# Kernel tuning notes

Measured on AMD Instinct MI355X. Metric: run time of the kernel, lower is better.

The kernel has to match this reference:

```python
import jax, jax.numpy as jnp
import numpy as np
from jax import lax

B, T, D = 256, 512, 256          # batch, time, input_dim (neurons)
HE, HC, HG = 256, 256, 256       # encoder/controller/generator hidden
L, F = 64, 64                    # latent_dim, factor_dim


def gru_cell(x, h, Wih, Whh, bih, bhh):
    # PyTorch GRU gate order: r, z, n
    gi = x @ Wih.T + bih
    gh = h @ Whh.T + bhh
    ir, iz, inn = jnp.split(gi, 3, axis=-1)
    hr, hz, hn = jnp.split(gh, 3, axis=-1)
    r = jax.nn.sigmoid(ir + hr)
    z = jax.nn.sigmoid(iz + hz)
    n = jnp.tanh(inn + r * hn)
    return (1.0 - z) * n + z * h


def setup_inputs() -> dict:
    key = jax.random.key(0)
    ks = iter(jax.random.split(key, 40))
    def p(shape, scale=0.05):
        return (jax.random.normal(next(ks), shape, dtype=jnp.float32) * scale)
    inp = {
        "x": jax.random.normal(next(ks), (B, T, D), dtype=jnp.float32),
        "eps_u": jax.random.normal(next(ks), (T, B, L), dtype=jnp.float32),
        # bidirectional encoder GRU (forward / backward directions)
        "Wih_ef": p((3 * HE, D)), "Whh_ef": p((3 * HE, HE)), "bih_ef": p((3 * HE,)), "bhh_ef": p((3 * HE,)),
        "Wih_eb": p((3 * HE, D)), "Whh_eb": p((3 * HE, HE)), "bih_eb": p((3 * HE,)), "bhh_eb": p((3 * HE,)),
        # initial-condition heads
        "W_mu0": p((L, 2 * HE)), "b_mu0": p((L,)), "W_lv0": p((L, 2 * HE)), "b_lv0": p((L,)),
        # controller GRU + heads
        "Wih_c": p((3 * HC, D + F)), "Whh_c": p((3 * HC, HC)), "bih_c": p((3 * HC,)), "bhh_c": p((3 * HC,)),
        "W_cmu": p((L, HC)), "b_cmu": p((L,)), "W_clv": p((L, HC)), "b_clv": p((L,)),
        # generator GRU
        "Wih_g": p((3 * HG, L)), "Whh_g": p((3 * HG, HG)), "bih_g": p((3 * HG,)), "bhh_g": p((3 * HG,)),
        # readouts
        "W_f": p((F, HG)), "b_f": p((F,)), "W_r": p((D, F)), "b_r": p((D,)),
    }
    return inp


def reference(x, eps_u, Wih_ef, Whh_ef, bih_ef, bhh_ef, Wih_eb, Whh_eb, bih_eb, bhh_eb,
              W_mu0, b_mu0, W_lv0, b_lv0, Wih_c, Whh_c, bih_c, bhh_c,
              W_cmu, b_cmu, W_clv, b_clv, Wih_g, Whh_g, bih_g, bhh_g,
              W_f, b_f, W_r, b_r):
    xt = jnp.transpose(x, (1, 0, 2))  # [T, B, D]
    h0 = jnp.zeros((x.shape[0], HE), dtype=x.dtype)

    def enc_f(h, x_t):
        return gru_cell(x_t, h, Wih_ef, Whh_ef, bih_ef, bhh_ef), None

    def enc_b(h, x_t):
        return gru_cell(x_t, h, Wih_eb, Whh_eb, bih_eb, bhh_eb), None

    h_fwd, _ = lax.scan(enc_f, h0, xt)
    h_bwd, _ = lax.scan(enc_b, h0, xt, reverse=True)
    h_enc = jnp.concatenate([h_fwd, h_bwd], axis=-1)  # [B, 2*HE]

    mu0 = h_enc @ W_mu0.T + b_mu0
    lv0 = h_enc @ W_lv0.T + b_lv0
    kl_ics = (0.5 * jnp.sum(jnp.exp(lv0) + mu0 ** 2 - 1.0 - lv0, axis=1)).mean()
    # note: z0 is sampled in the original but never used (generator starts from zeros)

    c0 = jnp.zeros((x.shape[0], HC), dtype=x.dtype)
    g0 = jnp.zeros((x.shape[0], HG), dtype=x.dtype)
    f0 = jnp.zeros((x.shape[0], F), dtype=x.dtype)

    def step(carry, inputs):
        c_h, g_h, prev_f = carry
        x_t, eps_t = inputs
        c_in = jnp.concatenate([x_t, prev_f], axis=-1)  # [B, D+F]
        c_h = gru_cell(c_in, c_h, Wih_c, Whh_c, bih_c, bhh_c)
        mu_u = c_h @ W_cmu.T + b_cmu
        lv_u = c_h @ W_clv.T + b_clv
        u_t = mu_u + eps_t * jnp.exp(0.5 * lv_u)
        kl_t = (0.5 * jnp.sum(jnp.exp(lv_u) + mu_u ** 2 - 1.0 - lv_u, axis=1)).mean()
        g_h = gru_cell(u_t, g_h, Wih_g, Whh_g, bih_g, bhh_g)
        factors = g_h @ W_f.T + b_f
        rates_t = jnp.exp(factors @ W_r.T + b_r)
        return (c_h, g_h, factors), (rates_t, factors, kl_t)

    _, (rates, factors_all, kl_ts) = lax.scan(step, (c0, g0, f0), (xt, eps_u))
    rates = jnp.transpose(rates, (1, 0, 2))           # [B, T, D]
    factors_all = jnp.transpose(factors_all, (1, 0, 2))  # [B, T, F]
    kl_ctrl = kl_ts.mean()  # sum of per-step means / T
    return (rates, kl_ics, kl_ctrl, factors_all)
```

## Files before the change

### kernel.cpp

```cpp
#include <hip/hip_runtime.h>

typedef unsigned char u8;
typedef unsigned short u16;
typedef unsigned int u32;
typedef unsigned long long u64;
typedef short short8 __attribute__((ext_vector_type(8)));
typedef __bf16 bf16x8 __attribute__((ext_vector_type(8)));
typedef float f32x4 __attribute__((ext_vector_type(4)));
typedef float f32x2 __attribute__((ext_vector_type(2)));
typedef long longx2 __attribute__((ext_vector_type(2)));

#define DEV static __device__ __forceinline__

struct Params {
  const float *x, *eps;
  const float *Wih_ef, *Whh_ef, *bih_ef, *bhh_ef;
  const float *Wih_eb, *Whh_eb, *bih_eb, *bhh_eb;
  const float *W_mu0, *b_mu0, *W_lv0, *b_lv0;
  const float *Wih_c, *Whh_c, *bih_c, *bhh_c;
  const float *W_cmu, *b_cmu, *W_clv, *b_clv;
  const float *Wih_g, *Whh_g, *bih_g, *bhh_g;
  const float *W_f, *b_f, *W_r, *b_r;
  u8  *Xf8;
  u16 *ebf;
  u16 *wihcbf;
  float *bfc;
  u8 *wihef8, *whhef8, *wiheb8, *whheb8;
  u8 *whhc8, *whhg8;
  u8 *wihcf8, *wihg8;
  u8 *wf8, *wcmu8, *wclv8;
  u16 *wrbf;
  float *cbn;
  float *gb;
  float *hdb;
  float *fb2;
  float *eb;
  float *henc;
  float *klacc;
  float *klics;
  u8 *Gxc;
  float *out;
};

constexpr size_t RATES_N = 33554432ull;
constexpr size_t FOUT    = RATES_N + 2ull;

DEV u16 f2bf(float x) {
  unsigned u = __builtin_bit_cast(unsigned, x);
  u = (u + 0x7FFFu + ((u >> 16) & 1u)) >> 16;
  return (u16)u;
}
DEV float bf2f(u32 s) { return __builtin_bit_cast(float, s << 16); }
DEV unsigned f2e4m3(float x) {
  unsigned u = __builtin_bit_cast(unsigned, x);
  unsigned s = (u >> 24) & 0x80u;
  float ax = __builtin_bit_cast(float, u & 0x7FFFFFFFu);
  if (ax > 448.f) return s | 0x7E;
  if (ax < 0.0009765625f) return s;
  if (ax < 0.015625f) {
    int m = (int)rintf(ax * 512.f);
    if (m >= 8) return s | 0x08;
    return s | (unsigned)m;
  }
  unsigned au = __builtin_bit_cast(unsigned, ax);
  int E = (int)(au >> 23) - 127;
  unsigned m = au & 0x7FFFFFu;
  unsigned r = (m + 0x7FFFFu + ((m >> 20) & 1u)) >> 20;
  if (r >= 8) { r = 0; ++E; if (E > 8) return s | 0x7E; }
// ... 48 lines not shown
}
DEV short8 ldfrag(const u16* p0, int stride) {
  const int l = threadIdx.x & 63;
  const u16* p = p0 + (size_t)(l & 15) * stride + ((l >> 4) << 3);
  return *reinterpret_cast<const short8*>(p);
}
DEV short8 ldfrag_f32(const float* p0, int stride) {
  const int l = threadIdx.x & 63;
  const float* p = p0 + (size_t)(l & 15) * stride + ((l >> 4) << 3);
  f32x4 a = *reinterpret_cast<const f32x4*>(p);
  f32x4 b = *reinterpret_cast<const f32x4*>(p + 4);
  short8 r;
  r[0]=(short)f2bf(a[0]); r[1]=(short)f2bf(a[1]); r[2]=(short)f2bf(a[2]); r[3]=(short)f2bf(a[3]);
  r[4]=(short)f2bf(b[0]); r[5]=(short)f2bf(b[1]); r[6]=(short)f2bf(b[2]); r[7]=(short)f2bf(b[3]);
  return r;
}
DEV longx2 ldws2(const u8* w, int tile, int p) {
  return *(const longx2*)(w + ((size_t)tile << 12) + (p << 10) + ((threadIdx.x & 63) << 4));
}
DEV longx2 ldws64x(const u8* w, int tile) {
  return *(const longx2*)(w + ((size_t)tile << 10) + ((threadIdx.x & 63) << 4));
}
DEV int fragoff(int row, int jb) { return jb * 128 + ((row ^ (jb & 15)) << 3); }
DEV long ldsF(const u8* m, int r0, int rs, int kk) {
  int l = threadIdx.x & 63;
  int jb = kk * 4 + (l >> 4);
  return *(const long*)(m + ((r0 >> 4) << (rs + 4)) + fragoff(l & 15, jb));
}
DEV void stF(u8* m, int row, int col, unsigned v) {
  *(unsigned*)(m + fragoff(row, col >> 3) + (col & 7)) = v;
}
DEV short8 ldsB16(const u8* m, int r0, int kk) {
  int l = threadIdx.x & 63;
  int row = r0 + (l & 15);
  int off = row * 512 + kk * 64 + ((l >> 4) << 4);
  off ^= (row & 7) << 4;
  return *(const short8*)(m + off);
}
DEV void stage16(u8* dst, const u8* src, int nbytes) {
  for (int i = threadIdx.x * 16; i < nbytes; i += blockDim.x * 16) {
    int row = i >> 9;
    int off = i ^ ((row & 7) << 4);
    *(f32x4*)(dst + off) = *(const f32x4*)(src + i);
  }
}

__global__ __launch_bounds__(256) void k_init(Params P) {
  const size_t g  = (size_t)blockIdx.x * 256 + threadIdx.x;
  const size_t gs = (size_t)gridDim.x * 256;
  for (size_t i = g; i < 4194304ull; i += gs) {
    size_t flat = i << 3;
    int b = (int)(flat >> 17);
    int rem = (int)(flat & 131071);
    int t = rem >> 8, d = rem & 255;
    *(u64*)(P.Xf8 + (((size_t)t * 256 + b) << 8) + d) = pack8f8(P.x + flat);
  }
  for (size_t o = g; o < 1048576ull; o += gs) {
    int l = (int)(o & 63), k2 = (int)((o >> 6) & 1);
    int bt = (int)((o >> 7) & 15), t = (int)(o >> 11);
    int row = bt * 16 + (l & 15), col = k2 * 32 + ((l >> 4) << 3);
    const float* s = P.eps + ((size_t)t * 256 + row) * 64 + col;
    f32x4 v0 = *(const f32x4*)s, v1 = *(const f32x4*)(s + 4);
    short8 ob;
    ob[0]=(short)f2bf(v0[0]); ob[1]=(short)f2bf(v0[1]); ob[2]=(short)f2bf(v0[2]); ob[3]=(short)f2bf(v0[3]);
    ob[4]=(short)f2bf(v1[0]); ob[5]=(short)f2bf(v1[1]); ob[6]=(short)f2bf(v1[2]); ob[7]=(short)f2bf(v1[3]);
    *(short8*)((u8*)P.ebf + o * 16) = ob;
  }
  const int gi = (int)g, gsi = (int)gs;
  for (int i = gi; i < 24576; i += gsi) {
    int l = i & 63, kk = (i >> 6) & 7, tile = i >> 9;
    int row = tile * 16 + (l & 15), col = kk * 32 + ((l >> 4) << 3);
    size_t so = (size_t)row * 256 + col;
    size_t db = ((size_t)tile << 12) + ((kk >> 1) << 10) + (l << 4) + ((kk & 1) << 3);
    *(u64*)(P.whhc8  + db) = pack8f8(P.Whh_c  + so);
    *(u64*)(P.whhg8  + db) = pack8f8(P.Whh_g  + so);
    *(u64*)(P.wihef8 + db) = pack8f8(P.Wih_ef + so);
    *(u64*)(P.whhef8 + db) = pack8f8(P.Whh_ef + so);
    *(u64*)(P.wiheb8 + db) = pack8f8(P.Wih_eb + so);
    *(u64*)(P.whheb8 + db) = pack8f8(P.Whh_eb + so);
  }
  for (int i = gi; i < 2048; i += gsi) {
    int l = i & 63, kk = (i >> 6) & 7, tile = i >> 9;
    int row = tile * 16 + (l & 15), col = kk * 32 + ((l >> 4) << 3);
    size_t so = (size_t)row * 256 + col;
    size_t db = ((size_t)tile << 12) + ((kk >> 1) << 10) + (l << 4) + ((kk & 1) << 3);
    *(u64*)(P.wf8   + db) = pack8f8(P.W_f   + so);
    *(u64*)(P.wcmu8 + db) = pack8f8(P.W_cmu + so);
    *(u64*)(P.wclv8 + db) = pack8f8(P.W_clv + so);
  }
  for (int i = gi; i < 6144; i += gsi) {
    int l = i & 63, k2 = (i >> 6) & 1, tile = i >> 7;
    int row = tile * 16 + (l & 15), col = k2 * 32 + ((l >> 4) << 3);
    size_t db = ((size_t)tile << 10) + (l << 4) + (k2 << 3);
    *(u64*)(P.wihcf8 + db) = pack8f8(P.Wih_c + (size_t)row * 320 + 256 + col);
    *(u64*)(P.wihg8  + db) = pack8f8(P.Wih_g + (size_t)row * 64 + col);
  }
  for (int i = gi; i < 196608; i += gsi) {
    int r = i >> 8, c = i & 255;
    P.wihcbf[i] = f2bf(P.Wih_c[r * 320 + c]);
  }
  for (int i = gi; i < 16384; i += gsi) P.wrbf[i] = f2bf(P.W_r[i]);
  for (int i = gi; i < 768; i += gsi)
    P.bfc[i] = P.bih_c[i] + (i < 512 ? P.bhh_c[i] : 0.f);
  for (int i = gi; i < 256; i += gsi) {
    P.cbn[i] = P.bhh_c[512 + i];
    P.gb[i]        = P.bih_g[i] + P.bhh_g[i];
    P.gb[256 + i]  = P.bih_g[256 + i] + P.bhh_g[256 + i];
    P.gb[512 + i]  = P.bih_g[512 + i];
    P.gb[768 + i]  = P.bhh_g[512 + i];
    P.eb[i]        = P.bih_ef[i] + P.bhh_ef[i];
    P.eb[256 + i]  = P.bih_ef[256 + i] + P.bhh_ef[256 + i];
    P.eb[512 + i]  = P.bih_ef[512 + i];
    P.eb[768 + i]  = P.bhh_ef[512 + i];
    P.eb[1024 + i] = P.bih_eb[i] + P.bhh_eb[i];
    P.eb[1280 + i] = P.bih_eb[256 + i] + P.bhh_eb[256 + i];
    P.eb[1536 + i] = P.bih_eb[512 + i];
    P.eb[1792 + i] = P.bhh_eb[512 + i];
  }
  for (int i = gi; i < 128; i += gsi) P.hdb[i] = (i < 64) ? P.b_cmu[i] : P.b_clv[i - 64];
  for (int i = gi; i < 64; i += gsi)  P.fb2[i] = P.b_f[i];
}

__global__ __launch_bounds__(512, 2) void k_gx(Params P) {
  extern __shared__ char smem[];
  u8* sA = (u8*)smem;
  u8* sB = sA + 65536;
  const int nc = blockIdx.x % 6;
  const int tb = blockIdx.x / 6;
  const int t = tb >> 1, bh = tb & 1;
  stage16(sA, (const u8*)(P.wihcbf + (size_t)nc * 128 * 256), 65536);
  for (int i = threadIdx.x * 8; i < 32768; i += 512 * 8) {
    int r = i >> 8, c = i & 255;
    const float* s = P.x + ((size_t)(bh * 128 + r) * 512 + t) * 256 + c;
    f32x4 v0 = *(const f32x4*)s, v1 = *(const f32x4*)(s + 4);
    short8 o;
    o[0]=(short)f2bf(v0[0]); o[1]=(short)f2bf(v0[1]); o[2]=(short)f2bf(v0[2]); o[3]=(short)f2bf(v0[3]);
    o[4]=(short)f2bf(v1[0]); o[5]=(short)f2bf(v1[1]); o[6]=(short)f2bf(v1[2]); o[7]=(short)f2bf(v1[3]);
    int off = (r * 512 + c * 2) ^ ((r & 7) << 4);
    *(short8*)(sB + off) = o;
  }
  __syncthreads();
  const int lane = threadIdx.x & 63, wid = threadIdx.x >> 6;
  const int rq = (lane >> 4) << 2;
  const int nglob = nc * 128 + wid * 16;
  short8 Af[8];
  #pragma unroll
  for (int kk = 0; kk < 8; ++kk) Af[kk] = ldsB16(sA, wid * 16, kk);
  float bq[4];
  #pragma unroll
  for (int q = 0; q < 4; ++q) bq[q] = P.bfc[nglob + rq + q];
  #pragma unroll 1
  for (int bt = 0; bt < 8; ++bt) {
    f32x4 acc = {0.f, 0.f, 0.f, 0.f};
    #pragma unroll
    for (int kk = 0; kk < 8; ++kk)
      acc = MFMA(Af[kk], ldsB16(sB, bt * 16, kk), acc);
    float v0 = acc[0] + bq[0], v1 = acc[1] + bq[1], v2 = acc[2] + bq[2], v3 = acc[3] + bq[3];
    unsigned pw = pk2fp8<false>(v0, v1, 0u); pw = pk2fp8<true>(v2, v3, pw);
    *(u32*)(P.Gxc + (((size_t)(t * 16 + bh * 8 + bt) * 48 + (nglob >> 4)) << 8) + (lane << 2)) = pw;
  }
}

DEV void cg_role(const Params& P, int blk, char* smem) {
  u8* hc8  = (u8*)smem;
  u8* hg8  = hc8 + 8192;
  u8* f8b  = hg8 + 8192;
  float* sml  = (float*)(f8b + 2048);
  float* sred = sml + 16 * 132;

  const int lane = threadIdx.x & 63, wid = threadIdx.x >> 6;
  const int cl = lane & 15, rq = (lane >> 4) << 2;
  const int b0 = blk << 4, j0 = wid << 5, jt = wid << 1;
  const int sel = wid >> 2, l0 = (wid & 3) << 4;

  for (int i = threadIdx.x * 4; i < 18432; i += 512 * 4) *(int*)(hc8 + i) = 0;

  f32x4 bnv[2], brv[2], bzv[2], biv[2], bhv2[2];
  #pragma unroll
  for (int c2 = 0; c2 < 2; ++c2) {
    int j = j0 + c2 * 16 + rq;
    bnv[c2]  = *(const f32x4*)(P.cbn + j);
    brv[c2]  = *(const f32x4*)(P.gb + j);
    bzv[c2]  = *(const f32x4*)(P.gb + 256 + j);
    biv[c2]  = *(const f32x4*)(P.gb + 512 + j);
    bhv2[c2] = *(const f32x4*)(P.gb + 768 + j);
  }
  f32x4 hbv = *(const f32x4*)(P.hdb + sel * 64 + l0 + rq);
  f32x4 fbv = {0, 0, 0, 0};
  if (wid < 4) fbv = *(const f32x4*)(P.fb2 + wid * 16 + rq);

  f32x4 hcM[2] = {{0,0,0,0},{0,0,0,0}};
  f32x4 hgM[2] = {{0,0,0,0},{0,0,0,0}};
  float klv = 0.f;
  __syncthreads();

  #pragma unroll 1
  for (int t = 0; t < 512; ++t) {
    const int cur = t & 1, prv = cur ^ 1;
    u8 *hcP = hc8 + prv * 4096, *hcC = hc8 + cur * 4096;
    u8 *hgP = hg8 + prv * 4096, *hgC = hg8 + cur * 4096;
    int zz = 0; asm volatile("" : "+v"(zz));
    const u8* wcS = P.whhc8 + zz;
    const u8* wgS = P.whhg8 + zz;
    const u8* cfS = P.wihcf8 + zz;
    const u8* guS = P.wihg8 + zz;
    const u8* hdS = (sel ? P.wclv8 : P.wcmu8) + zz;
    const u8* wfS = P.wf8 + zz;
    u32 gx[6];
    { const u8* gp = P.Gxc + (((size_t)(t * 16 + blk) * 48) << 8) + (lane << 2);
      #pragma unroll
      for (int c2 = 0; c2 < 2; ++c2)
        #pragma unroll
        for (int g3 = 0; g3 < 3; ++g3)
          gx[c2 * 3 + g3] = *(const u32*)(gp + ((g3 * 16 + jt + c2) << 8));
    }
    short8 ee0 = *(const short8*)((const u8*)P.ebf + (((size_t)(t * 16 + blk) * 2 + 0) << 10) + lane * 16);
    short8 ee1 = *(const short8*)((const u8*)P.ebf + (((size_t)(t * 16 + blk) * 2 + 1) << 10) + lane * 16);
    long hf[8];
    #pragma unroll
    for (int kk = 0; kk < 8; ++kk) hf[kk] = ldsF(hcP, 0, 8, kk);
    long ff0 = ldsF(f8b + prv * 1024, 0, 6, 0);
    long ff1 = ldsF(f8b + prv * 1024, 0, 6, 1);
    #pragma unroll
    for (int c2 = 0; c2 < 2; ++c2) {
      longx2 w0[4], w1[4], w2[4];
      #pragma unroll
      for (int p = 0; p < 4; ++p) {
        w0[p] = ldws2(wcS,      jt + c2, p);
        w1[p] = ldws2(wcS, 16 + jt + c2, p);
        w2[p] = ldws2(wcS, 32 + jt + c2, p);
      }
      longx2 cf0 = ldws64x(cfS,      jt + c2);
      longx2 cf1 = ldws64x(cfS, 16 + jt + c2);
      longx2 cf2 = ldws64x(cfS, 32 + jt + c2);
      f32x4 ar = {0,0,0,0}, az = {0,0,0,0}, ai = {0,0,0,0}, ah = {0,0,0,0};
      #pragma unroll
      for (int p = 0; p < 4; ++p) {
        ar = mfma8(w0[p].x, hf[2*p], ar);  ar = mfma8(w0[p].y, hf[2*p+1], ar);
        az = mfma8(w1[p].x, hf[2*p], az);  az = mfma8(w1[p].y, hf[2*p+1], az);
        ah = mfma8(w2[p].x, hf[2*p], ah);  ah = mfma8(w2[p].y, hf[2*p+1], ah);
      }
      ar = mfma8(cf0.x, ff0, ar); ar = mfma8(cf0.y, ff1, ar);
      az = mfma8(cf1.x, ff0, az); az = mfma8(cf1.y, ff1, az);
      ai = mfma8(cf2.x, ff0, ai); ai = mfma8(cf2.y, ff1, ai);
      f32x2 rlo = pkf32<false>(gx[c2*3+0]), rhi = pkf32<true>(gx[c2*3+0]);
      f32x2 zlo = pkf32<false>(gx[c2*3+1]), zhi = pkf32<true>(gx[c2*3+1]);
      f32x2 nlo = pkf32<false>(gx[c2*3+2]), nhi = pkf32<true>(gx[c2*3+2]);
      f32x4 bn = bnv[c2];
      float h0 = gru_h(ar[0]+rlo[0], az[0]+zlo[0], ai[0]+nlo[0], ah[0]+bn[0], hcM[c2][0]);
      float h1 = gru_h(ar[1]+rlo[1], az[1]+zlo[1], ai[1]+nlo[1], ah[1]+bn[1], hcM[c2][1]);
      float h2 = gru_h(ar[2]+rhi[0], az[2]+zhi[0], ai[2]+nhi[0], ah[2]+bn[2], hcM[c2][2]);
      float h3 = gru_h(ar[3]+rhi[1], az[3]+zhi[1], ai[3]+nhi[1], ah[3]+bn[3], hcM[c2][3]);
      hcM[c2][0] = h0; hcM[c2][1] = h1; hcM[c2][2] = h2; hcM[c2][3] = h3;
      unsigned pw = pk2fp8<false>(h0, h1, 0u); pw = pk2fp8<true>(h2, h3, pw);
      stF(hcC, cl, j0 + c2 * 16 + rq, pw);
    }
    __syncthreads();
    { long hcv[8];
      #pragma unroll
      for (int kk = 0; kk < 8; ++kk) hcv[kk] = ldsF(hcC, 0, 8, kk);
      f32x4 am = {0,0,0,0};
      #pragma unroll
      for (int p = 0; p < 4; ++p) {
        longx2 wp = ldws2(hdS, wid & 3, p);
        am = mfma8(wp.x, hcv[2*p], am);
        am = mfma8(wp.y, hcv[2*p+1], am);
      }
      am += hbv;
      *(f32x4*)(sml + cl * 132 + sel * 64 + l0 + rq) = am;
    }
    __syncthreads();
    long U[2];
    { const float* ml = sml + cl * 132;
      const int kh = (lane >> 4) << 3;
      #pragma unroll
      for (int k2 = 0; k2 < 2; ++k2) {
        f32x4 mu0 = *(const f32x4*)(ml + k2 * 32 + kh);
        f32x4 mu1 = *(const f32x4*)(ml + k2 * 32 + kh + 4);
        f32x4 lv0 = *(const f32x4*)(ml + 64 + k2 * 32 + kh);
        f32x4 lv1 = *(const f32x4*)(ml + 64 + k2 * 32 + kh + 4);
        short8 ev = k2 ? ee1 : ee0;
        float uu[8];
        #pragma unroll
        for (int e = 0; e < 4; ++e) {
          float epv = bf2f((u32)(u16)ev[e]);
          uu[e] = mu0[e] + epv * __expf(0.5f * lv0[e]);
        }
        #pragma unroll
        for (int e = 0; e < 4; ++e) {
          float epv = bf2f((u32)(u16)ev[4 + e]);
          uu[4 + e] = mu1[e] + epv * __expf(0.5f * lv1[e]);
        }
        unsigned pa = pk2fp8<false>(uu[0], uu[1], 0u); pa = pk2fp8<true>(uu[2], uu[3], pa);
        unsigned pb = pk2fp8<false>(uu[4], uu[5], 0u); pb = pk2fp8<true>(uu[6], uu[7], pb);
        U[k2] = (long)(((u64)pb << 32) | (u64)pa);
      }
    }
    long hg[8];
    #pragma unroll
    for (int kk = 0; kk < 8; ++kk) hg[kk] = ldsF(hgP, 0, 8, kk);
    #pragma unroll
    for (int c2 = 0; c2 < 2; ++c2) {
      longx2 g0[4], g1[4], g2[4];
      #pragma unroll
      for (int p = 0; p < 4; ++p) {
        g0[p] = ldws2(wgS,      jt + c2, p);
        g1[p] = ldws2(wgS, 16 + jt + c2, p);
        g2[p] = ldws2(wgS, 32 + jt + c2, p);
      }
      longx2 u0 = ldws64x(guS,      jt + c2);
      longx2 u1 = ldws64x(guS, 16 + jt + c2);
      longx2 u2 = ldws64x(guS, 32 + jt + c2);
      f32x4 gr = {0,0,0,0}, gz = {0,0,0,0}, gi = {0,0,0,0}, gh = {0,0,0,0};
      #pragma unroll
      for (int p = 0; p < 4; ++p) {
        gr = mfma8(g0[p].x, hg[2*p], gr);  gr = mfma8(g0[p].y, hg[2*p+1], gr);
        gz = mfma8(g1[p].x, hg[2*p], gz);  gz = mfma8(g1[p].y, hg[2*p+1], gz);
        gh = mfma8(g2[p].x, hg[2*p], gh);  gh = mfma8(g2[p].y, hg[2*p+1], gh);
      }
      gr = mfma8(u0.x, U[0], gr); gr = mfma8(u0.y, U[1], gr);
      gz = mfma8(u1.x, U[0], gz); gz = mfma8(u1.y, U[1], gz);
      gi = mfma8(u2.x, U[0], gi); gi = mfma8(u2.y, U[1], gi);
      float h0 = gru_h(gr[0]+brv[c2][0], gz[0]+bzv[c2][0], gi[0]+biv[c2][0], gh[0]+bhv2[c2][0], hgM[c2][0]);
      float h1 = gru_h(gr[1]+brv[c2][1], gz[1]+bzv[c2][1], gi[1]+biv[c2][1], gh[1]+bhv2[c2][1], hgM[c2][1]);
      float h2 = gru_h(gr[2]+brv[c2][2], gz[2]+bzv[c2][2], gi[2]+biv[c2][2], gh[2]+bhv2[c2][2], hgM[c2][2]);
      float h3 = gru_h(gr[3]+brv[c2][3], gz[3]+bzv[c2][3], gi[3]+biv[c2][3], gh[3]+bhv2[c2][3], hgM[c2][3]);
      hgM[c2][0] = h0; hgM[c2][1] = h1; hgM[c2][2] = h2; hgM[c2][3] = h3;
      unsigned pw = pk2fp8<false>(h0, h1, 0u); pw = pk2fp8<true>(h2, h3, pw);
      stF(hgC, cl, j0 + c2 * 16 + rq, pw);
    }
    __syncthreads();
    if (wid < 4) {
      long hgv[8];
      #pragma unroll
      for (int kk = 0; kk < 8; ++kk) hgv[kk] = ldsF(hgC, 0, 8, kk);
      f32x4 af = {0,0,0,0};
      #pragma unroll
      for (int p = 0; p < 4; ++p) {
        longx2 wp = ldws2(wfS, wid, p);
        af = mfma8(wp.x, hgv[2*p], af);
        af = mfma8(wp.y, hgv[2*p+1], af);
      }
      af += fbv;
      float* fo = P.out + FOUT + (size_t)(b0 + cl) * 32768 + (size_t)t * 64 + wid * 16 + rq;
      f32x2 lo = {af[0], af[1]}, hi2 = {af[2], af[3]};
      *(f32x2*)fo = lo;
      *(f32x2*)(fo + 2) = hi2;
      unsigned pw = pk2fp8<false>(af[0], af[1], 0u); pw = pk2fp8<true>(af[2], af[3], pw);
      stF(f8b + cur * 1024, cl, wid * 16 + rq, pw);
    } else {
      #pragma unroll
      for (int e = 0; e < 4; ++e) {
        int p = ((wid - 4) * 64 + lane) * 4 + e;
        int row = p >> 6, l = p & 63;
        float mu = sml[row * 132 + l], lv = sml[row * 132 + 64 + l];
        klv += __expf(lv) + mu * mu - 1.f - lv;
      }
    }
    __syncthreads();
  }
  if (wid >= 4) {
    float v = klv;
    v += __shfl_down(v, 32); v += __shfl_down(v, 16); v += __shfl_down(v, 8);
    v += __shfl_down(v, 4);  v += __shfl_down(v, 2);  v += __shfl_down(v, 1);
    if (lane == 0) sred[wid] = v;
  }
  __syncthreads();
  if (threadIdx.x == 0) P.klacc[blk] = sred[4] + sred[5] + sred[6] + sred[7];
}

DEV void enc_role(const Params& P, int dir, int b0, char* smem) {
  u8* h8 = (u8*)smem;
  u8* sx = h8 + 8192;
  const int lane = threadIdx.x & 63, wid = threadIdx.x >> 6;
  const int cl = lane & 15, rq = (lane >> 4) << 2;
  const int j0 = wid << 5, jt = wid << 1;
  const u8* wihS0 = dir ? P.wiheb8 : P.wihef8;
  const u8* whhS0 = dir ? P.whheb8 : P.whhef8;
  const float* ebt = P.eb + dir * 1024;
  for (int i = threadIdx.x * 4; i < 8192; i += 512 * 4) *(int*)(h8 + i) = 0;
  f32x4 brv[2], bzv[2], biv[2], bhv2[2];
  #pragma unroll
  for (int c2 = 0; c2 < 2; ++c2) {
    int j = j0 + c2 * 16 + rq;
    brv[c2]  = *(const f32x4*)(ebt + j);
    bzv[c2]  = *(const f32x4*)(ebt + 256 + j);
    biv[c2]  = *(const f32x4*)(ebt + 512 + j);
    bhv2[c2] = *(const f32x4*)(ebt + 768 + j);
  }
  f32x4 heM[2] = {{0,0,0,0},{0,0,0,0}};
  const int ssrc = threadIdx.x * 8;
  const int sdst = fragoff(threadIdx.x >> 5, threadIdx.x & 31);
  const int t0 = dir ? 511 : 0;
  *(u64*)(sx + sdst) = *(const u64*)(P.Xf8 + (((size_t)t0 * 256 + b0) << 8) + ssrc);
  __syncthreads();

  #pragma unroll 1
  for (int i = 0; i < 512; ++i) {
    const int cur = i & 1, prv = cur ^ 1;
    const int t = dir ? (511 - i) : i;
    u8 *hP = h8 + prv * 4096, *hC = h8 + cur * 4096;
    const u8* sxc = sx + cur * 4096;
    int zz = 0; asm volatile("" : "+v"(zz));
    const u8* wihS = wihS0 + zz;
    const u8* whhS = whhS0 + zz;
    u64 xpre = 0;
    if (i < 511) {
      int tn = dir ? (t - 1) : (t + 1);
      xpre = *(const u64*)(P.Xf8 + (((size_t)tn * 256 + b0) << 8) + ssrc);
    }
    long hp[8], xv[8];
    #pragma unroll
    for (int kk = 0; kk < 8; ++kk) { hp[kk] = ldsF(hP, 0, 8, kk); xv[kk] = ldsF(sxc, 0, 8, kk); }
    #pragma unroll
    for (int c2 = 0; c2 < 2; ++c2) {
      longx2 H0[4], H1[4], H2[4], I0[4], I1[4], I2[4];
      #pragma unroll
      for (int p = 0; p < 4; ++p) {
        H0[p] = ldws2(whhS,      jt + c2, p);
        H1[p] = ldws2(whhS, 16 + jt + c2, p);
        H2[p] = ldws2(whhS, 32 + jt + c2, p);
        I0[p] = ldws2(wihS,      jt + c2, p);
        I1[p] = ldws2(wihS, 16 + jt + c2, p);
        I2[p] = ldws2(wihS, 32 + jt + c2, p);
      }
      f32x4 er = {0,0,0,0}, ez = {0,0,0,0}, ei = {0,0,0,0}, eh = {0,0,0,0};
      #pragma unroll
      for (int p = 0; p < 4; ++p) {
        er = mfma8(H0[p].x, hp[2*p], er);  er = mfma8(H0[p].y, hp[2*p+1], er);
        ez = mfma8(H1[p].x, hp[2*p], ez);  ez = mfma8(H1[p].y, hp[2*p+1], ez);
        eh = mfma8(H2[p].x, hp[2*p], eh);  eh = mfma8(H2[p].y, hp[2*p+1], eh);
        er = mfma8(I0[p].x, xv[2*p], er);  er = mfma8(I0[p].y, xv[2*p+1], er);
        ez = mfma8(I1[p].x, xv[2*p], ez);  ez = mfma8(I1[p].y, xv[2*p+1], ez);
        ei = mfma8(I2[p].x, xv[2*p], ei);  ei = mfma8(I2[p].y, xv[2*p+1], ei);
      }
      float h0 = gru_h(er[0]+brv[c2][0], ez[0]+bzv[c2][0], ei[0]+biv[c2][0], eh[0]+bhv2[c2][0], heM[c2][0]);
      float h1 = gru_h(er[1]+brv[c2][1], ez[1]+bzv[c2][1], ei[1]+biv[c2][1], eh[1]+bhv2[c2][1], heM[c2][1]);
      float h2 = gru_h(er[2]+brv[c2][2], ez[2]+bzv[c2][2], ei[2]+biv[c2][2], eh[2]+bhv2[c2][2], heM[c2][2]);
      float h3 = gru_h(er[3]+brv[c2][3], ez[3]+bzv[c2][3], ei[3]+biv[c2][3], eh[3]+bhv2[c2][3], heM[c2][3]);
      heM[c2][0] = h0; heM[c2][1] = h1; heM[c2][2] = h2; heM[c2][3] = h3;
      unsigned pw = pk2fp8<false>(h0, h1, 0u); pw = pk2fp8<true>(h2, h3, pw);
      stF(hC, cl, j0 + c2 * 16 + rq, pw);
    }
    if (i < 511) *(u64*)(sx + prv * 4096 + sdst) = xpre;
    __syncthreads();
  }
  #pragma unroll
  for (int c2 = 0; c2 < 2; ++c2)
    *(f32x4*)(P.henc + (size_t)(dir * 256 + b0 + cl) * 256 + j0 + c2 * 16 + rq) = heM[c2];
}

__global__ __launch_bounds__(512, 2) void k_main(Params P) {
  extern __shared__ char smem[];
  const int blk = blockIdx.x;
  if (blk < 16) cg_role(P, blk, smem);
  else {
    const int e = blk - 16;
    enc_role(P, e >> 4, (e & 15) << 4, smem);
  }
}

__global__ __launch_bounds__(256) void k_post(Params P) {
  const int blk = blockIdx.x;
  if (blk < 32) {
    __shared__ float red[4];
    float ka = 0.f;
    #pragma unroll 1
    for (int pp = 0; pp < 2; ++pp) {
      int p = blk * 512 + threadIdx.x * 2 + pp;
      int b = p >> 6, l = p & 63;
      float mu = P.b_mu0[l], lv = P.b_lv0[l];
      const float* wm = P.W_mu0 + (size_t)l * 512;
      const float* wl = P.W_lv0 + (size_t)l * 512;
      const float* h0 = P.henc + (size_t)b * 256;
      const float* h1 = P.henc + (size_t)(256 + b) * 256;
      #pragma unroll 4
      for (int k = 0; k < 256; ++k) {
        float hf = h0[k], hb = h1[k];
        mu += hf * wm[k] + hb * wm[256 + k];
        lv += hf * wl[k] + hb * wl[256 + k];
      }
// ... 22 lines not shown
      a = MFMA(ldfrag(W + 32, 64), F1, a);
      f32x4 rb = *(const f32x4*)(P.b_r + d0 + rq);
      f32x4 o;
      o[0] = __expf(a[0] + rb[0]); o[1] = __expf(a[1] + rb[1]);
      o[2] = __expf(a[2] + rb[2]); o[3] = __expf(a[3] + rb[3]);
      *(f32x4*)(P.out + (r0 + cl) * 256 + d0 + rq) = o;
    }
  }
}

__global__ void k_final(Params P) {
  if (threadIdx.x == 0) {
    float s = 0.f, s2 = 0.f;
    for (int i = 0; i < 16; ++i) s += P.klacc[i];
    for (int i = 0; i < 32; ++i) s2 += P.klics[i];
    P.out[RATES_N]     = s2 * (0.5f / 256.f);
    P.out[RATES_N + 1] = s  * (0.5f / (256.f * 512.f));
  }
}

extern "C" void kernel_launch(void* const* d_in, const int* in_sizes, int n_in,
                              void* d_out, int out_size, void* d_ws, size_t ws_size,
                              hipStream_t stream) {
  (void)in_sizes; (void)n_in; (void)out_size; (void)ws_size;
  Params P;
  const float* const* in = (const float* const*)d_in;
  P.x = in[0];      P.eps = in[1];
  P.Wih_ef = in[2]; P.Whh_ef = in[3]; P.bih_ef = in[4]; P.bhh_ef = in[5];
  P.Wih_eb = in[6]; P.Whh_eb = in[7]; P.bih_eb = in[8]; P.bhh_eb = in[9];
  P.W_mu0 = in[10]; P.b_mu0 = in[11]; P.W_lv0 = in[12]; P.b_lv0 = in[13];
  P.Wih_c = in[14]; P.Whh_c = in[15]; P.bih_c = in[16]; P.bhh_c = in[17];
  P.W_cmu = in[18]; P.b_cmu = in[19]; P.W_clv = in[20]; P.b_clv = in[21];
  P.Wih_g = in[22]; P.Whh_g = in[23]; P.bih_g = in[24]; P.bhh_g = in[25];
  P.W_f = in[26];   P.b_f = in[27];   P.W_r = in[28];   P.b_r = in[29];

  char* w = (char*)d_ws;
  size_t off = 0;
  auto take = [&](size_t bytes) -> char* {
    char* r = w + off;
    off = (off + bytes + 255) & ~(size_t)255;
    return r;
  };
  P.Xf8    = (u8*)take(33554432ull);
  P.ebf    = (u16*)take(16777216ull * 2);
  P.wihcbf = (u16*)take(196608ull * 2);
  P.bfc    = (float*)take(768ull * 4);
  P.wihef8 = (u8*)take(196608ull);
  P.whhef8 = (u8*)take(196608ull);
  P.wiheb8 = (u8*)take(196608ull);
  P.whheb8 = (u8*)take(196608ull);
  P.whhc8  = (u8*)take(196608ull);
  P.whhg8  = (u8*)take(196608ull);
  P.wihcf8 = (u8*)take(49152ull);
  P.wihg8  = (u8*)take(49152ull);
  P.wf8    = (u8*)take(16384ull);
  P.wcmu8  = (u8*)take(16384ull);
  P.wclv8  = (u8*)take(16384ull);
  P.wrbf   = (u16*)take(16384ull * 2);
  P.cbn    = (float*)take(256ull * 4);
  P.gb     = (float*)take(1024ull * 4);
  P.hdb    = (float*)take(128ull * 4);
  P.fb2    = (float*)take(64ull * 4);
  P.eb     = (float*)take(2048ull * 4);
  P.henc   = (float*)take(131072ull * 4);
  P.klacc  = (float*)take(64ull * 4);
  P.klics  = (float*)take(64ull * 4);
  P.Gxc    = (u8*)d_out;
  P.out    = (float*)d_out;

  hipLaunchKernelGGL(k_init,  dim3(2048), dim3(256), 0, stream, P);
  hipLaunchKernelGGL(k_gx,    dim3(6144), dim3(512), 131072, stream, P);
  hipLaunchKernelGGL(k_main,  dim3(48),   dim3(512), 27008, stream, P);
  hipLaunchKernelGGL(k_post,  dim3(2080), dim3(256), 0, stream, P);
  hipLaunchKernelGGL(k_final, dim3(1),    dim3(64),  0, stream, P);
}
```

Baseline: 4.712 ms.

## Precompute encoder input projections in k_gx and stage recurrent weights in LDS

```diff
diff --git a/kernel.cpp b/kernel.cpp
--- a/kernel.cpp
+++ b/kernel.cpp
@@ -23,14 +23,16 @@
   const float *W_f, *b_f, *W_r, *b_r;
   u8  *Xf8;
   u16 *ebf;
-  u16 *wihcbf;
+  u16 *wihcbf, *wihefbf, *wihebbf;
   float *bfc;
+  float *bfe;
   u8 *wihef8, *whhef8, *wiheb8, *whheb8;
   u8 *whhc8, *whhg8;
   u8 *wihcf8, *wihg8;
   u8 *wf8, *wcmu8, *wclv8;
   u16 *wrbf;
   float *cbn;
+  float *ebn;
   float *gb;
   float *hdb;
   float *fb2;
@@ -39,11 +41,14 @@
   float *klacc;
   float *klics;
   u8 *Gxc;
+  u8 *Gxe;
+  int useGxe;
   float *out;
 };
 
 constexpr size_t RATES_N = 33554432ull;
 constexpr size_t FOUT    = RATES_N + 2ull;
+constexpr size_t GXE_D   = 100663296ull;
 
 DEV u16 f2bf(float x) {
   unsigned u = __builtin_bit_cast(unsigned, x);
@@ -138,10 +143,15 @@
   return *(const longx2*)(w + ((size_t)tile << 10) + ((threadIdx.x & 63) << 4));
 }
 DEV int fragoff(int row, int jb) { return jb * 128 + ((row ^ (jb & 15)) << 3); }
-DEV long ldsF(const u8* m, int r0, int rs, int kk) {
+DEV long ldsF(const u8* m, int kk) {
   int l = threadIdx.x & 63;
   int jb = kk * 4 + (l >> 4);
-  return *(const long*)(m + ((r0 >> 4) << (rs + 4)) + fragoff(l & 15, jb));
+  return *(const long*)(m + fragoff(l & 15, jb));
+}
+DEV long ldsF64(const u8* m, int k2) {
+  int l = threadIdx.x & 63;
+  int jb = k2 * 4 + (l >> 4);
+  return *(const long*)(m + fragoff(l & 15, jb));
 }
 DEV void stF(u8* m, int row, int col, unsigned v) {
   *(unsigned*)(m + fragoff(row, col >> 3) + (col & 7)) = v;
@@ -160,16 +170,22 @@
     *(f32x4*)(dst + off) = *(const f32x4*)(src + i);
   }
 }
+DEV void stageLin(u8* dst, const u8* src, int nbytes) {
+  for (int i = threadIdx.x * 16; i < nbytes; i += 512 * 16)
+    *(f32x4*)(dst + i) = *(const f32x4*)(src + i);
+}
 
 __global__ __launch_bounds__(256) void k_init(Params P) {
   const size_t g  = (size_t)blockIdx.x * 256 + threadIdx.x;
   const size_t gs = (size_t)gridDim.x * 256;
-  for (size_t i = g; i < 4194304ull; i += gs) {
-    size_t flat = i << 3;
-    int b = (int)(flat >> 17);
-    int rem = (int)(flat & 131071);
-    int t = rem >> 8, d = rem & 255;
-    *(u64*)(P.Xf8 + (((size_t)t * 256 + b) << 8) + d) = pack8f8(P.x + flat);
+  if (!P.useGxe) {
+    for (size_t i = g; i < 4194304ull; i += gs) {
+      size_t flat = i << 3;
+      int b = (int)(flat >> 17);
+      int rem = (int)(flat & 131071);
+      int t = rem >> 8, d = rem & 255;
+      *(u64*)(P.Xf8 + (((size_t)t * 256 + b) << 8) + d) = pack8f8(P.x + flat);
+    }
   }
   for (size_t o = g; o < 1048576ull; o += gs) {
     int l = (int)(o & 63), k2 = (int)((o >> 6) & 1);
@@ -213,13 +229,20 @@
   }
   for (int i = gi; i < 196608; i += gsi) {
     int r = i >> 8, c = i & 255;
-    P.wihcbf[i] = f2bf(P.Wih_c[r * 320 + c]);
+    P.wihcbf[i]  = f2bf(P.Wih_c[r * 320 + c]);
+    P.wihefbf[i] = f2bf(P.Wih_ef[i]);
+    P.wihebbf[i] = f2bf(P.Wih_eb[i]);
   }
   for (int i = gi; i < 16384; i += gsi) P.wrbf[i] = f2bf(P.W_r[i]);
-  for (int i = gi; i < 768; i += gsi)
+  for (int i = gi; i < 768; i += gsi) {
     P.bfc[i] = P.bih_c[i] + (i < 512 ? P.bhh_c[i] : 0.f);
+    P.bfe[i]       = P.bih_ef[i] + (i < 512 ? P.bhh_ef[i] : 0.f);
+    P.bfe[768 + i] = P.bih_eb[i] + (i < 512 ? P.bhh_eb[i] : 0.f);
+  }
   for (int i = gi; i < 256; i += gsi) {
     P.cbn[i] = P.bhh_c[512 + i];
+    P.ebn[i]       = P.bhh_ef[512 + i];
+    P.ebn[256 + i] = P.bhh_eb[512 + i];
     P.gb[i]        = P.bih_g[i] + P.bhh_g[i];
     P.gb[256 + i]  = P.bih_g[256 + i] + P.bhh_g[256 + i];
     P.gb[512 + i]  = P.bih_g[512 + i];
@@ -241,10 +264,15 @@
   extern __shared__ char smem[];
   u8* sA = (u8*)smem;
   u8* sB = sA + 65536;
-  const int nc = blockIdx.x % 6;
-  const int tb = blockIdx.x / 6;
+  const int mm = blockIdx.x / 6144;
+  const int bb = blockIdx.x % 6144;
+  const int nc = bb % 6;
+  const int tb = bb / 6;
   const int t = tb >> 1, bh = tb & 1;
-  stage16(sA, (const u8*)(P.wihcbf + (size_t)nc * 128 * 256), 65536);
+  const u16* Abf = (mm == 0) ? P.wihcbf : ((mm == 1) ? P.wihefbf : P.wihebbf);
+  const float* bias = (mm == 0) ? P.bfc : (P.bfe + (mm - 1) * 768);
+  u8* dst = (mm == 0) ? P.Gxc : (P.Gxe + (size_t)(mm - 1) * GXE_D);
+  stage16(sA, (const u8*)(Abf + (size_t)nc * 128 * 256), 65536);
   for (int i = threadIdx.x * 8; i < 32768; i += 512 * 8) {
     int r = i >> 8, c = i & 255;
     const float* s = P.x + ((size_t)(bh * 128 + r) * 512 + t) * 256 + c;
@@ -264,7 +292,7 @@
   for (int kk = 0; kk < 8; ++kk) Af[kk] = ldsB16(sA, wid * 16, kk);
   float bq[4];
   #pragma unroll
-  for (int q = 0; q < 4; ++q) bq[q] = P.bfc[nglob + rq + q];
+  for (int q = 0; q < 4; ++q) bq[q] = bias[nglob + rq + q];
   #pragma unroll 1
   for (int bt = 0; bt < 8; ++bt) {
     f32x4 acc = {0.f, 0.f, 0.f, 0.f};
@@ -273,12 +301,15 @@
       acc = MFMA(Af[kk], ldsB16(sB, bt * 16, kk), acc);
     float v0 = acc[0] + bq[0], v1 = acc[1] + bq[1], v2 = acc[2] + bq[2], v3 = acc[3] + bq[3];
     unsigned pw = pk2fp8<false>(v0, v1, 0u); pw = pk2fp8<true>(v2, v3, pw);
-    *(u32*)(P.Gxc + (((size_t)(t * 16 + bh * 8 + bt) * 48 + (nglob >> 4)) << 8) + (lane << 2)) = pw;
+    *(u32*)(dst + (((size_t)(t * 16 + bh * 8 + bt) * 48 + (nglob >> 4)) << 8) + (lane << 2)) = pw;
   }
 }
 
 DEV void cg_role(const Params& P, int blk, char* smem) {
-  u8* hc8  = (u8*)smem;
+  u8* sWcf = (u8*)smem;
+  u8* sWg  = sWcf + 49152;
+  u8* sWhd = sWg + 49152;
+  u8* hc8  = sWhd + 32768;
   u8* hg8  = hc8 + 8192;
   u8* f8b  = hg8 + 8192;
   float* sml  = (float*)(f8b + 2048);
@@ -289,6 +320,10 @@
   const int b0 = blk << 4, j0 = wid << 5, jt = wid << 1;
   const int sel = wid >> 2, l0 = (wid & 3) << 4;
 
+  stageLin(sWcf, P.wihcf8, 49152);
+  stageLin(sWg,  P.wihg8,  49152);
+  stageLin(sWhd, P.wcmu8, 16384);
+  stageLin(sWhd + 16384, P.wclv8, 16384);
   for (int i = threadIdx.x * 4; i < 18432; i += 512 * 4) *(int*)(hc8 + i) = 0;
 
   f32x4 bnv[2], brv[2], bzv[2], biv[2], bhv2[2];
@@ -303,7 +338,7 @@
   }
   f32x4 hbv = *(const f32x4*)(P.hdb + sel * 64 + l0 + rq);
   f32x4 fbv = {0, 0, 0, 0};
-  if (wid < 4) fbv = *(const f32x4*)(P.fb2 + wid * 16 + rq);
+  if (wid < 4) fbv = *(const f32x4*)(P.fb2 + (wid << 4) + rq);
 
   f32x4 hcM[2] = {{0,0,0,0},{0,0,0,0}};
   f32x4 hgM[2] = {{0,0,0,0},{0,0,0,0}};
@@ -315,13 +350,6 @@
     const int cur = t & 1, prv = cur ^ 1;
     u8 *hcP = hc8 + prv * 4096, *hcC = hc8 + cur * 4096;
     u8 *hgP = hg8 + prv * 4096, *hgC = hg8 + cur * 4096;
-    int zz = 0; asm volatile("" : "+v"(zz));
-    const u8* wcS = P.whhc8 + zz;
-    const u8* wgS = P.whhg8 + zz;
-    const u8* cfS = P.wihcf8 + zz;
-    const u8* guS = P.wihg8 + zz;
-    const u8* hdS = (sel ? P.wclv8 : P.wcmu8) + zz;
-    const u8* wfS = P.wf8 + zz;
     u32 gx[6];
     { const u8* gp = P.Gxc + (((size_t)(t * 16 + blk) * 48) << 8) + (lane << 2);
       #pragma unroll
@@ -334,21 +362,21 @@
     short8 ee1 = *(const short8*)((const u8*)P.ebf + (((size_t)(t * 16 + blk) * 2 + 1) << 10) + lane * 16);
     long hf[8];
     #pragma unroll
-    for (int kk = 0; kk < 8; ++kk) hf[kk] = ldsF(hcP, 0, 8, kk);
-    long ff0 = ldsF(f8b + prv * 1024, 0, 6, 0);
-    long ff1 = ldsF(f8b + prv * 1024, 0, 6, 1);
+    for (int kk = 0; kk < 8; ++kk) hf[kk] = ldsF(hcP, kk);
+    long ff0 = ldsF64(f8b + prv * 1024, 0);
+    long ff1 = ldsF64(f8b + prv * 1024, 1);
     #pragma unroll
     for (int c2 = 0; c2 < 2; ++c2) {
       longx2 w0[4], w1[4], w2[4];
       #pragma unroll
       for (int p = 0; p < 4; ++p) {
-        w0[p] = ldws2(wcS,      jt + c2, p);
-        w1[p] = ldws2(wcS, 16 + jt + c2, p);
-        w2[p] = ldws2(wcS, 32 + jt + c2, p);
-      }
-      longx2 cf0 = ldws64x(cfS,      jt + c2);
-      longx2 cf1 = ldws64x(cfS, 16 + jt + c2);
-      longx2 cf2 = ldws64x(cfS, 32 + jt + c2);
+        w0[p] = ldws2(P.whhc8,      jt + c2, p);
+        w1[p] = ldws2(P.whhc8, 16 + jt + c2, p);
+        w2[p] = ldws2(P.whhc8, 32 + jt + c2, p);
+      }
+      longx2 cf0 = ldws64x(sWcf,      jt + c2);
+      longx2 cf1 = ldws64x(sWcf, 16 + jt + c2);
+      longx2 cf2 = ldws64x(sWcf, 32 + jt + c2);
       f32x4 ar = {0,0,0,0}, az = {0,0,0,0}, ai = {0,0,0,0}, ah = {0,0,0,0};
       #pragma unroll
       for (int p = 0; p < 4; ++p) {
@@ -374,11 +402,11 @@
     __syncthreads();
     { long hcv[8];
       #pragma unroll
-      for (int kk = 0; kk < 8; ++kk) hcv[kk] = ldsF(hcC, 0, 8, kk);
+      for (int kk = 0; kk < 8; ++kk) hcv[kk] = ldsF(hcC, kk);
       f32x4 am = {0,0,0,0};
       #pragma unroll
       for (int p = 0; p < 4; ++p) {
-        longx2 wp = ldws2(hdS, wid & 3, p);
+        longx2 wp = ldws2(sWhd + sel * 16384, wid & 3, p);
         am = mfma8(wp.x, hcv[2*p], am);
         am = mfma8(wp.y, hcv[2*p+1], am);
       }
@@ -414,19 +442,19 @@
     }
     long hg[8];
     #pragma unroll
-    for (int kk = 0; kk < 8; ++kk) hg[kk] = ldsF(hgP, 0, 8, kk);
+    for (int kk = 0; kk < 8; ++kk) hg[kk] = ldsF(hgP, kk);
     #pragma unroll
     for (int c2 = 0; c2 < 2; ++c2) {
       longx2 g0[4], g1[4], g2[4];
       #pragma unroll
       for (int p = 0; p < 4; ++p) {
-        g0[p] = ldws2(wgS,      jt + c2, p);
-        g1[p] = ldws2(wgS, 16 + jt + c2, p);
-        g2[p] = ldws2(wgS, 32 + jt + c2, p);
-      }
-      longx2 u0 = ldws64x(guS,      jt + c2);
-      longx2 u1 = ldws64x(guS, 16 + jt + c2);
-      longx2 u2 = ldws64x(guS, 32 + jt + c2);
+        g0[p] = ldws2(P.whhg8,      jt + c2, p);
+        g1[p] = ldws2(P.whhg8, 16 + jt + c2, p);
+        g2[p] = ldws2(P.whhg8, 32 + jt + c2, p);
+      }
+      longx2 u0 = ldws64x(sWg,      jt + c2);
+      longx2 u1 = ldws64x(sWg, 16 + jt + c2);
+      longx2 u2 = ldws64x(sWg, 32 + jt + c2);
       f32x4 gr = {0,0,0,0}, gz = {0,0,0,0}, gi = {0,0,0,0}, gh = {0,0,0,0};
       #pragma unroll
       for (int p = 0; p < 4; ++p) {
@@ -449,11 +477,11 @@
     if (wid < 4) {
       long hgv[8];
       #pragma unroll
-      for (int kk = 0; kk < 8; ++kk) hgv[kk] = ldsF(hgC, 0, 8, kk);
+      for (int kk = 0; kk < 8; ++kk) hgv[kk] = ldsF(hgC, kk);
       f32x4 af = {0,0,0,0};
       #pragma unroll
       for (int p = 0; p < 4; ++p) {
-        longx2 wp = ldws2(wfS, wid, p);
+        longx2 wp = ldws2(P.wf8, wid, p);
         af = mfma8(wp.x, hgv[2*p], af);
         af = mfma8(wp.y, hgv[2*p+1], af);
       }
@@ -485,30 +513,41 @@
   if (threadIdx.x == 0) P.klacc[blk] = sred[4] + sred[5] + sred[6] + sred[7];
 }
 
+template <bool GXE>
 DEV void enc_role(const Params& P, int dir, int b0, char* smem) {
-  u8* h8 = (u8*)smem;
-  u8* sx = h8 + 8192;
+  u8* sWhh = (u8*)smem;
+  u8* h8   = sWhh + 131072;
+  u8* sx   = h8 + 8192;
   const int lane = threadIdx.x & 63, wid = threadIdx.x >> 6;
   const int cl = lane & 15, rq = (lane >> 4) << 2;
   const int j0 = wid << 5, jt = wid << 1;
-  const u8* wihS0 = dir ? P.wiheb8 : P.wihef8;
-  const u8* whhS0 = dir ? P.whheb8 : P.whhef8;
-  const float* ebt = P.eb + dir * 1024;
+  const int btile = b0 >> 4;
+  const u8* wihG = dir ? P.wiheb8 : P.wihef8;
+  const u8* whhG = dir ? P.whheb8 : P.whhef8;
+  stageLin(sWhh, whhG, 131072);
   for (int i = threadIdx.x * 4; i < 8192; i += 512 * 4) *(int*)(h8 + i) = 0;
-  f32x4 brv[2], bzv[2], biv[2], bhv2[2];
+  f32x4 bnv[2], brv[2], bzv[2], biv[2], bhv2[2];
   #pragma unroll
   for (int c2 = 0; c2 < 2; ++c2) {
     int j = j0 + c2 * 16 + rq;
-    brv[c2]  = *(const f32x4*)(ebt + j);
-    bzv[c2]  = *(const f32x4*)(ebt + 256 + j);
-    biv[c2]  = *(const f32x4*)(ebt + 512 + j);
-    bhv2[c2] = *(const f32x4*)(ebt + 768 + j);
+    if (GXE) {
+      bnv[c2] = *(const f32x4*)(P.ebn + dir * 256 + j);
+    } else {
+      const float* ebt = P.eb + dir * 1024;
+      brv[c2]  = *(const f32x4*)(ebt + j);
+      bzv[c2]  = *(const f32x4*)(ebt + 256 + j);
+      biv[c2]  = *(const f32x4*)(ebt + 512 + j);
+      bhv2[c2] = *(const f32x4*)(ebt + 768 + j);
+    }
   }
   f32x4 heM[2] = {{0,0,0,0},{0,0,0,0}};
   const int ssrc = threadIdx.x * 8;
-  const int sdst = fragoff(threadIdx.x >> 5, threadIdx.x & 31);
-  const int t0 = dir ? 511 : 0;
-  *(u64*)(sx + sdst) = *(const u64*)(P.Xf8 + (((size_t)t0 * 256 + b0) << 8) + ssrc);
+  const int sdst = fragoff(threadIdx.x >> 5, threadIdx.x & 31) + ((threadIdx.x >> 5) >> 4 ? 0 : 0);
+  if (!GXE) {
+    const int t0 = dir ? 511 : 0;
+    *(u64*)(sx + fragoff(threadIdx.x >> 5, threadIdx.x & 31)) =
+        *(const u64*)(P.Xf8 + (((size_t)t0 * 256 + b0) << 8) + ssrc);
+  }
   __syncthreads();
 
   #pragma unroll 1
@@ -516,49 +555,82 @@
     const int cur = i & 1, prv = cur ^ 1;
     const int t = dir ? (511 - i) : i;
     u8 *hP = h8 + prv * 4096, *hC = h8 + cur * 4096;
+    u32 gx[6];
+    u64 xpre = 0;
     const u8* sxc = sx + cur * 4096;
-    int zz = 0; asm volatile("" : "+v"(zz));
-    const u8* wihS = wihS0 + zz;
-    const u8* whhS = whhS0 + zz;
-    u64 xpre = 0;
-    if (i < 511) {
-      int tn = dir ? (t - 1) : (t + 1);
-      xpre = *(const u64*)(P.Xf8 + (((size_t)tn * 256 + b0) << 8) + ssrc);
-    }
-    long hp[8], xv[8];
+    if (GXE) {
+      const u8* gp = P.Gxe + (size_t)dir * GXE_D +
+                     (((size_t)(t * 16 + btile) * 48) << 8) + (lane << 2);
+      #pragma unroll
+      for (int c2 = 0; c2 < 2; ++c2)
+        #pragma unroll
+        for (int g3 = 0; g3 < 3; ++g3)
+          gx[c2 * 3 + g3] = *(const u32*)(gp + ((g3 * 16 + jt + c2) << 8));
+    } else {
+      if (i < 511) {
+        int tn = dir ? (t - 1) : (t + 1);
+        xpre = *(const u64*)(P.Xf8 + (((size_t)tn * 256 + b0) << 8) + ssrc);
+      }
+    }
+    long hp[8];
     #pragma unroll
-    for (int kk = 0; kk < 8; ++kk) { hp[kk] = ldsF(hP, 0, 8, kk); xv[kk] = ldsF(sxc, 0, 8, kk); }
+    for (int kk = 0; kk < 8; ++kk) hp[kk] = ldsF(hP, kk);
     #pragma unroll
     for (int c2 = 0; c2 < 2; ++c2) {
-      longx2 H0[4], H1[4], H2[4], I0[4], I1[4], I2[4];
+      longx2 Hr[4], Hz[4], Hn[4];
       #pragma unroll
       for (int p = 0; p < 4; ++p) {
-        H0[p] = ldws2(whhS,      jt + c2, p);
-        H1[p] = ldws2(whhS, 16 + jt + c2, p);
-        H2[p] = ldws2(whhS, 32 + jt + c2, p);
-        I0[p] = ldws2(wihS,      jt + c2, p);
-        I1[p] = ldws2(wihS, 16 + jt + c2, p);
-        I2[p] = ldws2(wihS, 32 + jt + c2, p);
+        Hr[p] = ldws2(sWhh,      jt + c2, p);
+        Hz[p] = ldws2(sWhh, 16 + jt + c2, p);
+        Hn[p] = ldws2(whhG, 32 + jt + c2, p);
       }
       f32x4 er = {0,0,0,0}, ez = {0,0,0,0}, ei = {0,0,0,0}, eh = {0,0,0,0};
       #pragma unroll
       for (int p = 0; p < 4; ++p) {
-        er = mfma8(H0[p].x, hp[2*p], er);  er = mfma8(H0[p].y, hp[2*p+1], er);
-        ez = mfma8(H1[p].x, hp[2*p], ez);  ez = mfma8(H1[p].y, hp[2*p+1], ez);
-        eh = mfma8(H2[p].x, hp[2*p], eh);  eh = mfma8(H2[p].y, hp[2*p+1], eh);
-        er = mfma8(I0[p].x, xv[2*p], er);  er = mfma8(I0[p].y, xv[2*p+1], er);
-        ez = mfma8(I1[p].x, xv[2*p], ez);  ez = mfma8(I1[p].y, xv[2*p+1], ez);
-        ei = mfma8(I2[p].x, xv[2*p], ei);  ei = mfma8(I2[p].y, xv[2*p+1], ei);
-      }
-      float h0 = gru_h(er[0]+brv[c2][0], ez[0]+bzv[c2][0], ei[0]+biv[c2][0], eh[0]+bhv2[c2][0], heM[c2][0]);
-      float h1 = gru_h(er[1]+brv[c2][1], ez[1]+bzv[c2][1], ei[1]+biv[c2][1], eh[1]+bhv2[c2][1], heM[c2][1]);
-      float h2 = gru_h(er[2]+brv[c2][2], ez[2]+bzv[c2][2], ei[2]+biv[c2][2], eh[2]+bhv2[c2][2], heM[c2][2]);
-      float h3 = gru_h(er[3]+brv[c2][3], ez[3]+bzv[c2][3], ei[3]+biv[c2][3], eh[3]+bhv2[c2][3], heM[c2][3]);
+        er = mfma8(Hr[p].x, hp[2*p], er);  er = mfma8(Hr[p].y, hp[2*p+1], er);
+        ez = mfma8(Hz[p].x, hp[2*p], ez);  ez = mfma8(Hz[p].y, hp[2*p+1], ez);
+        eh = mfma8(Hn[p].x, hp[2*p], eh);  eh = mfma8(Hn[p].y, hp[2*p+1], eh);
+      }
+      if (!GXE) {
+        long xv[8];
+        #pragma unroll
+        for (int kk = 0; kk < 8; ++kk) xv[kk] = ldsF(sxc, kk);
+        longx2 Ir[4], Iz[4], In[4];
+        #pragma unroll
+        for (int p = 0; p < 4; ++p) {
+          Ir[p] = ldws2(wihG,      jt + c2, p);
+          Iz[p] = ldws2(wihG, 16 + jt + c2, p);
+          In[p] = ldws2(wihG, 32 + jt + c2, p);
+        }
+        #pragma unroll
+        for (int p = 0; p < 4; ++p) {
+          er = mfma8(Ir[p].x, xv[2*p], er);  er = mfma8(Ir[p].y, xv[2*p+1], er);
+          ez = mfma8(Iz[p].x, xv[2*p], ez);  ez = mfma8(Iz[p].y, xv[2*p+1], ez);
+          ei = mfma8(In[p].x, xv[2*p], ei);  ei = mfma8(In[p].y, xv[2*p+1], ei);
+        }
+      }
+      float h0, h1, h2, h3;
+      if (GXE) {
+        f32x2 rlo = pkf32<false>(gx[c2*3+0]), rhi = pkf32<true>(gx[c2*3+0]);
+        f32x2 zlo = pkf32<false>(gx[c2*3+1]), zhi = pkf32<true>(gx[c2*3+1]);
+        f32x2 nlo = pkf32<false>(gx[c2*3+2]), nhi = pkf32<true>(gx[c2*3+2]);
+        f32x4 bn = bnv[c2];
+        h0 = gru_h(er[0]+rlo[0], ez[0]+zlo[0], nlo[0], eh[0]+bn[0], heM[c2][0]);
+        h1 = gru_h(er[1]+rlo[1], ez[1]+zlo[1], nlo[1], eh[1]+bn[1], heM[c2][1]);
+        h2 = gru_h(er[2]+rhi[0], ez[2]+zhi[0], nhi[0], eh[2]+bn[2], heM[c2][2]);
+        h3 = gru_h(er[3]+rhi[1], ez[3]+zhi[1], nhi[1], eh[3]+bn[3], heM[c2][3]);
+      } else {
+        h0 = gru_h(er[0]+brv[c2][0], ez[0]+bzv[c2][0], ei[0]+biv[c2][0], eh[0]+bhv2[c2][0], heM[c2][0]);
+        h1 = gru_h(er[1]+brv[c2][1], ez[1]+bzv[c2][1], ei[1]+biv[c2][1], eh[1]+bhv2[c2][1], heM[c2][1]);
+        h2 = gru_h(er[2]+brv[c2][2], ez[2]+bzv[c2][2], ei[2]+biv[c2][2], eh[2]+bhv2[c2][2], heM[c2][2]);
+        h3 = gru_h(er[3]+brv[c2][3], ez[3]+bzv[c2][3], ei[3]+biv[c2][3], eh[3]+bhv2[c2][3], heM[c2][3]);
+      }
       heM[c2][0] = h0; heM[c2][1] = h1; heM[c2][2] = h2; heM[c2][3] = h3;
       unsigned pw = pk2fp8<false>(h0, h1, 0u); pw = pk2fp8<true>(h2, h3, pw);
       stF(hC, cl, j0 + c2 * 16 + rq, pw);
     }
-    if (i < 511) *(u64*)(sx + prv * 4096 + sdst) = xpre;
+    if (!GXE && i < 511)
+      *(u64*)(sx + prv * 4096 + fragoff(threadIdx.x >> 5, threadIdx.x & 31)) = xpre;
     __syncthreads();
   }
   #pragma unroll
@@ -572,7 +644,8 @@
   if (blk < 16) cg_role(P, blk, smem);
   else {
     const int e = blk - 16;
-    enc_role(P, e >> 4, (e & 15) << 4, smem);
+    if (P.useGxe) enc_role<true>(P, e >> 4, (e & 15) << 4, smem);
+    else          enc_role<false>(P, e >> 4, (e & 15) << 4, smem);
   }
 }
 
@@ -641,7 +714,7 @@
 extern "C" void kernel_launch(void* const* d_in, const int* in_sizes, int n_in,
                               void* d_out, int out_size, void* d_ws, size_t ws_size,
                               hipStream_t stream) {
-  (void)in_sizes; (void)n_in; (void)out_size; (void)ws_size;
+  (void)in_sizes; (void)n_in; (void)out_size;
   Params P;
   const float* const* in = (const float* const*)d_in;
   P.x = in[0];      P.eps = in[1];
@@ -660,36 +733,43 @@
     off = (off + bytes + 255) & ~(size_t)255;
     return r;
   };
-  P.Xf8    = (u8*)take(33554432ull);
-  P.ebf    = (u16*)take(16777216ull * 2);
-  P.wihcbf = (u16*)take(196608ull * 2);
-  P.bfc    = (float*)take(768ull * 4);
-  P.wihef8 = (u8*)take(196608ull);
-  P.whhef8 = (u8*)take(196608ull);
-  P.wiheb8 = (u8*)take(196608ull);
-  P.whheb8 = (u8*)take(196608ull);
-  P.whhc8  = (u8*)take(196608ull);
-  P.whhg8  = (u8*)take(196608ull);
-  P.wihcf8 = (u8*)take(49152ull);
-  P.wihg8  = (u8*)take(49152ull);
-  P.wf8    = (u8*)take(16384ull);
-  P.wcmu8  = (u8*)take(16384ull);
-  P.wclv8  = (u8*)take(16384ull);
-  P.wrbf   = (u16*)take(16384ull * 2);
-  P.cbn    = (float*)take(256ull * 4);
-  P.gb     = (float*)take(1024ull * 4);
-  P.hdb    = (float*)take(128ull * 4);
-  P.fb2    = (float*)take(64ull * 4);
-  P.eb     = (float*)take(2048ull * 4);
-  P.henc   = (float*)take(131072ull * 4);
-  P.klacc  = (float*)take(64ull * 4);
-  P.klics  = (float*)take(64ull * 4);
-  P.Gxc    = (u8*)d_out;
-  P.out    = (float*)d_out;
+  P.Xf8     = (u8*)take(33554432ull);
+  P.ebf     = (u16*)take(16777216ull * 2);
+  P.wihcbf  = (u16*)take(196608ull * 2);
+  P.wihefbf = (u16*)take(196608ull * 2);
+  P.wihebbf = (u16*)take(196608ull * 2);
+  P.bfc     = (float*)take(768ull * 4);
+  P.bfe     = (float*)take(1536ull * 4);
+  P.wihef8  = (u8*)take(196608ull);
+  P.whhef8  = (u8*)take(196608ull);
+  P.wiheb8  = (u8*)take(196608ull);
+  P.whheb8  = (u8*)take(196608ull);
+  P.whhc8   = (u8*)take(196608ull);
+  P.whhg8   = (u8*)take(196608ull);
+  P.wihcf8  = (u8*)take(49152ull);
+  P.wihg8   = (u8*)take(49152ull);
+  P.wf8     = (u8*)take(16384ull);
+  P.wcmu8   = (u8*)take(16384ull);
+  P.wclv8   = (u8*)take(16384ull);
+  P.wrbf    = (u16*)take(16384ull * 2);
+  P.cbn     = (float*)take(256ull * 4);
+  P.ebn     = (float*)take(512ull * 4);
+  P.gb      = (float*)take(1024ull * 4);
+  P.hdb     = (float*)take(128ull * 4);
+  P.fb2     = (float*)take(64ull * 4);
+  P.eb      = (float*)take(2048ull * 4);
+  P.henc    = (float*)take(131072ull * 4);
+  P.klacc   = (float*)take(64ull * 4);
+  P.klics   = (float*)take(64ull * 4);
+  size_t gxe_off = (off + 255) & ~(size_t)255;
+  P.useGxe = (gxe_off + 2 * GXE_D <= ws_size) ? 1 : 0;
+  P.Gxe = P.useGxe ? (u8*)(w + gxe_off) : (u8*)w;
+  P.Gxc = (u8*)d_out;
+  P.out = (float*)d_out;
 
   hipLaunchKernelGGL(k_init,  dim3(2048), dim3(256), 0, stream, P);
-  hipLaunchKernelGGL(k_gx,    dim3(6144), dim3(512), 131072, stream, P);
-  hipLaunchKernelGGL(k_main,  dim3(48),   dim3(512), 27008, stream, P);
+  hipLaunchKernelGGL(k_gx,    dim3(P.useGxe ? 18432 : 6144), dim3(512), 131072, stream, P);
+  hipLaunchKernelGGL(k_main,  dim3(48),   dim3(512), 158016, stream, P);
   hipLaunchKernelGGL(k_post,  dim3(2080), dim3(256), 0, stream, P);
   hipLaunchKernelGGL(k_final, dim3(1),    dim3(64),  0, stream, P);
 }
```

After: 5.028 ms. +6.7%, slower.
